# Performance work log

Measured on AMD Instinct MI355X. Metric: run time of the kernel, lower is better.

The kernel has to match this reference:

```python
import jax, jax.numpy as jnp
import numpy as np

N_NODES = 100000
N_EDGES = 2000000
F_IN = 32
HID = 32
N_CLASS = 40


def _gru_cell(m, h, wih, whh, bih, bhh):
    # torch.nn.GRUCell math; wih/whh: [3H, H_in], gates ordered r, z, n
    gi = m @ wih.T + bih
    gh = h @ whh.T + bhh
    i_r, i_z, i_n = jnp.split(gi, 3, axis=-1)
    h_r, h_z, h_n = jnp.split(gh, 3, axis=-1)
    r = jax.nn.sigmoid(i_r + h_r)
    z = jax.nn.sigmoid(i_z + h_z)
    n = jnp.tanh(i_n + r * h_n)
    return (1.0 - z) * n + z * h


def _gated_conv(x, edge_index, edge_weight, w_proj, w_msg, wih, whh, bih, bhh):
    h = x @ w_proj                                   # [N, out]
    msg = (h @ w_msg)[edge_index[0]] * edge_weight[:, None]  # gather src -> [E, out]
    agg = jax.ops.segment_sum(msg, edge_index[1], num_segments=N_NODES)  # scatter-add to dst
    return _gru_cell(agg, h, wih, whh, bih, bhh)


def setup_inputs() -> dict:
    key = jax.random.key(0)
    ks = jax.random.split(key, 16)
    s = 0.1
    return {
        "x": jax.random.normal(ks[0], (N_NODES, F_IN), jnp.float32),
        "edge_index": jax.random.randint(ks[1], (2, N_EDGES), 0, N_NODES, jnp.int64),
        "edge_weight": jax.random.uniform(ks[2], (N_EDGES,), jnp.float32),
        "W1_proj": jax.random.normal(ks[3], (F_IN, HID), jnp.float32) * s,
        "W1_msg": jax.random.normal(ks[4], (HID, HID), jnp.float32) * s,
        "gru1_wih": jax.random.normal(ks[5], (3 * HID, HID), jnp.float32) * s,
        "gru1_whh": jax.random.normal(ks[6], (3 * HID, HID), jnp.float32) * s,
        "gru1_bih": jax.random.normal(ks[7], (3 * HID,), jnp.float32) * s,
        "gru1_bhh": jax.random.normal(ks[8], (3 * HID,), jnp.float32) * s,
        "W2_proj": jax.random.normal(ks[9], (HID, N_CLASS), jnp.float32) * s,
        "W2_msg": jax.random.normal(ks[10], (N_CLASS, N_CLASS), jnp.float32) * s,
        "gru2_wih": jax.random.normal(ks[11], (3 * N_CLASS, N_CLASS), jnp.float32) * s,
        "gru2_whh": jax.random.normal(ks[12], (3 * N_CLASS, N_CLASS), jnp.float32) * s,
        "gru2_bih": jax.random.normal(ks[13], (3 * N_CLASS,), jnp.float32) * s,
        "gru2_bhh": jax.random.normal(ks[14], (3 * N_CLASS,), jnp.float32) * s,
    }


def reference(x, edge_index, edge_weight, W1_proj, W1_msg, gru1_wih, gru1_whh,
              gru1_bih, gru1_bhh, W2_proj, W2_msg, gru2_wih, gru2_whh,
              gru2_bih, gru2_bhh):
    # eval mode: dropout is identity
    h = _gated_conv(x, edge_index, edge_weight, W1_proj, W1_msg,
                    gru1_wih, gru1_whh, gru1_bih, gru1_bhh)
    h = jax.nn.relu(h)
    h = _gated_conv(h, edge_index, edge_weight, W2_proj, W2_msg,
                    gru2_wih, gru2_whh, gru2_bih, gru2_bhh)
    return jax.nn.log_softmax(h, axis=-1)
```

## Files before the change

### kernel.cpp

```cpp
#include <hip/hip_runtime.h>
#include <math.h>

#define NN 100000
#define NP 100032
#define NE 2000000
#define FIN 32
#define H 32
#define NC 40

#define NBK 196
#define BSH 9
#define CAP 10880
#define EPT 16
#define EPB (256 * EPT)

#define NPROJ 12500
#define NWB 104

typedef _Float16 half_t;
typedef __attribute__((ext_vector_type(8))) _Float16 half8;
typedef __attribute__((ext_vector_type(4))) float f32x4;
typedef long long ll2 __attribute__((ext_vector_type(2)));

__device__ __forceinline__ float sigm_(float x) {
    return 1.0f / (1.0f + __expf(-x));
}
__device__ __forceinline__ float tanh_(float x) {
    x = fminf(fmaxf(x, -20.0f), 20.0f);
    float e = __expf(2.0f * x);
    return (e - 1.0f) / (e + 1.0f);
}

__device__ __forceinline__ void agg_run(int n, int q,
                                        const int* __restrict__ ofs,
                                        const int* __restrict__ ocn,
                                        const int2* __restrict__ evs,
                                        const half_t* __restrict__ src,
                                        float* acc) {
    const half8* s8 = (const half8*)src + q;
    const long long* ev8 = (const long long*)evs;
    int e = ofs[n];
    int e1 = e + ocn[n];
    if ((e & 1) && e < e1) {
        long long r = __builtin_nontemporal_load(ev8 + e);
        float w = __int_as_float((int)(r >> 32));
        half8 hv = s8[(size_t)(r & 0x1FFFF) * 4];
#pragma unroll
        for (int t = 0; t < 8; ++t) acc[t] += w * (float)hv[t];
        ++e;
    }
    for (; e + 8 <= e1; e += 8) {
        ll2 p0 = __builtin_nontemporal_load((const ll2*)(ev8 + e));
        ll2 p1 = __builtin_nontemporal_load((const ll2*)(ev8 + e + 2));
        ll2 p2 = __builtin_nontemporal_load((const ll2*)(ev8 + e + 4));
        ll2 p3 = __builtin_nontemporal_load((const ll2*)(ev8 + e + 6));
        half8 h0 = s8[(size_t)(p0[0] & 0x1FFFF) * 4];
        half8 h1 = s8[(size_t)(p0[1] & 0x1FFFF) * 4];
        half8 h2 = s8[(size_t)(p1[0] & 0x1FFFF) * 4];
        half8 h3 = s8[(size_t)(p1[1] & 0x1FFFF) * 4];
        half8 h4 = s8[(size_t)(p2[0] & 0x1FFFF) * 4];
        half8 h5 = s8[(size_t)(p2[1] & 0x1FFFF) * 4];
        half8 h6 = s8[(size_t)(p3[0] & 0x1FFFF) * 4];
        half8 h7 = s8[(size_t)(p3[1] & 0x1FFFF) * 4];
        float w0 = __int_as_float((int)(p0[0] >> 32));
        float w1 = __int_as_float((int)(p0[1] >> 32));
        float w2 = __int_as_float((int)(p1[0] >> 32));
        float w3 = __int_as_float((int)(p1[1] >> 32));
        float w4 = __int_as_float((int)(p2[0] >> 32));
        float w5 = __int_as_float((int)(p2[1] >> 32));
        float w6 = __int_as_float((int)(p3[0] >> 32));
        float w7 = __int_as_float((int)(p3[1] >> 32));
#pragma unroll
        for (int t = 0; t < 8; ++t) {
            acc[t] += w0 * (float)h0[t];
            acc[t] += w1 * (float)h1[t];
            acc[t] += w2 * (float)h2[t];
            acc[t] += w3 * (float)h3[t];
            acc[t] += w4 * (float)h4[t];
            acc[t] += w5 * (float)h5[t];
            acc[t] += w6 * (float)h6[t];
            acc[t] += w7 * (float)h7[t];
        }
    }
    if (e + 4 <= e1) {
        ll2 p0 = __builtin_nontemporal_load((const ll2*)(ev8 + e));
        ll2 p1 = __builtin_nontemporal_load((const ll2*)(ev8 + e + 2));
        half8 h0 = s8[(size_t)(p0[0] & 0x1FFFF) * 4];
        half8 h1 = s8[(size_t)(p0[1] & 0x1FFFF) * 4];
        half8 h2 = s8[(size_t)(p1[0] & 0x1FFFF) * 4];
        half8 h3 = s8[(size_t)(p1[1] & 0x1FFFF) * 4];
        float w0 = __int_as_float((int)(p0[0] >> 32));
        float w1 = __int_as_float((int)(p0[1] >> 32));
        float w2 = __int_as_float((int)(p1[0] >> 32));
        float w3 = __int_as_float((int)(p1[1] >> 32));
#pragma unroll
        for (int t = 0; t < 8; ++t) {
            acc[t] += w0 * (float)h0[t];
            acc[t] += w1 * (float)h1[t];
            acc[t] += w2 * (float)h2[t];
            acc[t] += w3 * (float)h3[t];
        }
        e += 4;
    }
    if (e + 2 <= e1) {
        ll2 p0 = __builtin_nontemporal_load((const ll2*)(ev8 + e));
        half8 h0 = s8[(size_t)(p0[0] & 0x1FFFF) * 4];
        half8 h1 = s8[(size_t)(p0[1] & 0x1FFFF) * 4];
        float w0 = __int_as_float((int)(p0[0] >> 32));
        float w1 = __int_as_float((int)(p0[1] >> 32));
#pragma unroll
        for (int t = 0; t < 8; ++t) {
            acc[t] += w0 * (float)h0[t];
            acc[t] += w1 * (float)h1[t];
        }
        e += 2;
    }
    if (e < e1) {
        long long r = __builtin_nontemporal_load(ev8 + e);
        float w = __int_as_float((int)(r >> 32));
        half8 hv = s8[(size_t)(r & 0x1FFFF) * 4];
#pragma unroll
        for (int t = 0; t < 8; ++t) acc[t] += w * (float)hv[t];
    }
}

__global__ __launch_bounds__(256) void kA_bucket(const int* __restrict__ ei,
                                                 const float* __restrict__ ew,
                                                 int* __restrict__ gcur,
                                                 long long* __restrict__ rec) {
    __shared__ long long recs[EPB];
    __shared__ int gdst[EPB];
    __shared__ int cnt[NBK], base[NBK], sofs[NBK];
    __shared__ int ssc[256];
    int tid = threadIdx.x;
    for (int i = tid; i < NBK; i += 256) cnt[i] = 0;
    __syncthreads();
    int e0 = blockIdx.x * EPB;
    int dcache[EPT];
#pragma unroll
    for (int i = 0; i < EPT; ++i) {
        int e = e0 + i * 256 + tid;
        dcache[i] = (e < NE) ? ei[NE + e] : -1;
        if (e < NE) atomicAdd(&cnt[dcache[i] >> BSH], 1);
    }
    __syncthreads();
    int cv = (tid < NBK) ? cnt[tid] : 0;
    ssc[tid] = cv;
    __syncthreads();
    for (int off = 1; off < 256; off <<= 1) {
        int v = (tid >= off) ? ssc[tid - off] : 0;
        __syncthreads();
        ssc[tid] += v;
        __syncthreads();
    }
    if (tid < NBK) {
        sofs[tid] = ssc[tid] - cv;
        base[tid] = atomicAdd(&gcur[tid], cv);
        cnt[tid] = 0;
    }
    __syncthreads();
#pragma unroll
    for (int i = 0; i < EPT; ++i) {
        int e = e0 + i * 256 + tid;
        if (e < NE) {
            int d = dcache[i], s = ei[e];
            int b = d >> BSH;
            int r = atomicAdd(&cnt[b], 1);
            int slot = sofs[b] + r;
            int pos = base[b] + r;
            int lo = s | ((d & 511) << 17);
            recs[slot] = (long long)(unsigned)lo |
                         ((long long)__float_as_int(ew[e]) << 32);
            gdst[slot] = (pos < CAP) ? (b * CAP + pos) : -1;
        }
    }
    __syncthreads();
    int nrec = min(EPB, NE - e0);
    for (int i = tid; i < nrec; i += 256) {
        int gd = gdst[i];
        if (gd >= 0) rec[gd] = recs[i];
    }
}

__global__ __launch_bounds__(256) void kB_sort(const int* __restrict__ gcur,
                                               const int2* __restrict__ rec,
                                               int2* __restrict__ evs,
                                               int* __restrict__ ofs,
                                               int* __restrict__ ocn) {
    __shared__ int hist[2048], lofs[2048], ssc[256];
    int tid = threadIdx.x, b = blockIdx.x;
    int nb0 = b << BSH;
    int nnodes = min(512, NN - nb0);
    int cntb = min(gcur[b], CAP);
    for (int i = tid; i < 2048; i += 256) hist[i] = 0;
    __syncthreads();
    const int2* rb = rec + (size_t)b * CAP;
    for (int i = tid; i < cntb; i += 256) {
        int rx = rb[i].x;
        int bin = (((rx >> 17) & 511) << 2) | ((rx & 0x1FFFF) >> 15);
        atomicAdd(&hist[bin], 1);
    }
    __syncthreads();
    int base = tid * 8, ls = 0, lh[8];
#pragma unroll
    for (int j = 0; j < 8; ++j) {
        lh[j] = hist[base + j];
        ls += lh[j];
    }
    ssc[tid] = ls;
    __syncthreads();
    for (int off = 1; off < 256; off <<= 1) {
        int v = (tid >= off) ? ssc[tid - off] : 0;
        __syncthreads();
        ssc[tid] += v;
        __syncthreads();
    }
    int ex = ssc[tid] - ls;
#pragma unroll
    for (int j = 0; j < 8; ++j) {
        lofs[base + j] = ex;
        ex += lh[j];
    }
    __syncthreads();
    for (int l = tid; l < nnodes; l += 256) {
        int c = hist[4 * l] + hist[4 * l + 1] + hist[4 * l + 2] + hist[4 * l + 3];
        ofs[nb0 + l] = b * CAP + lofs[4 * l];
        ocn[nb0 + l] = c;
    }
    __syncthreads();
    for (int i = tid; i < 2048; i += 256) hist[i] = 0;
    __syncthreads();
    int2* eb = evs + (size_t)b * CAP;
    for (int i = tid; i < cntb; i += 256) {
        int2 r = rb[i];
        int bin = (((r.x >> 17) & 511) << 2) | ((r.x & 0x1FFFF) >> 15);
        int rk = atomicAdd(&hist[bin], 1);
        eb[lofs[bin] + rk] = make_int2(r.x & 0x1FFFF, r.y);
    }
}

__global__ __launch_bounds__(256) void k_prep(const float* __restrict__ x,
                                              const float* __restrict__ W1p,
                                              const float* __restrict__ W1m,
                                              const float* __restrict__ wih1,
                                              const float* __restrict__ whh1,
                                              const float* __restrict__ W2p,
                                              const float* __restrict__ W2m,
                                              const float* __restrict__ wih2,
                                              const float* __restrict__ whh2,
                                              half_t* __restrict__ Hd,
                                              half_t* __restrict__ W1sw,
                                              half_t* __restrict__ W2sw,
                                              int* __restrict__ gcur) {
    __shared__ float sWp[FIN * H];
    __shared__ float sx[8][FIN];
    __shared__ float P2l[32 * NC];
    int b = blockIdx.x, tid = threadIdx.x;
    if (b < NPROJ) {
        for (int i = tid; i < FIN * H; i += 256) sWp[i] = W1p[i];
        int nb = b * 8;
        int nl = tid >> 5, j = tid & 31;
        int n = nb + nl;
        if (n < NN) sx[nl][j] = x[(size_t)n * FIN + j];
        __syncthreads();
        float acc = 0.f;
#pragma unroll
        for (int k = 0; k < FIN; ++k) acc += sx[nl][k] * sWp[k * H + j];
        if (n < NN) Hd[(size_t)n * 32 + j] = (half_t)acc;
        return;
    }
    int wb = b - NPROJ;
    if (wb == 0 && tid < NBK) gcur[tid] = 0;
    int i = wb * 256 + tid;
    if (i < 8192) {
        int j = i & 7, lane = (i >> 3) & 63, ct = (i >> 9) & 7, s = i >> 12;
        int k = s * 32 + (lane >> 4) * 8 + j;
        int col = ct * 16 + (lane & 15);
        int g = col >> 5, jj = col & 31;
        float v = 0.f;
        if (g <= 2) {
            if (k < 32) {
                float acc = 0.f;
#pragma unroll
                for (int t = 0; t < H; ++t) acc += W1m[k * H + t] * wih1[(g * H + jj) * H + t];
                v = acc;
            } else if (g < 2) {
                v = whh1[(g * H + jj) * H + (k - 32)];
            }
        } else {
            if (k >= 32) v = whh1[(2 * H + jj) * H + (k - 32)];
        }
        W1sw[i] = (half_t)v;
    } else {
        for (int e = tid; e < 32 * NC; e += 256) {
            int k = e / NC, t = e % NC;
            float a = 0.f;
#pragma unroll
            for (int u = 0; u < NC; ++u) a += W2p[k * NC + u] * W2m[u * NC + t];
            P2l[e] = a;
        }
        __syncthreads();
        int i2 = i - 8192;
        int j = i2 & 7, lane = (i2 >> 3) & 63;
        int tt = i2 >> 9;
        int ct = tt % 12, s = tt / 12;
        int k = s * 32 + (lane >> 4) * 8 + j;
        int col = ct * 16 + (lane & 15);
        int g = col / 48, jj = col % 48;
        float v = 0.f;
        if (jj < NC) {
            if (g <= 2) {
                if (k < 32) {
                    float acc = 0.f;
#pragma unroll
                    for (int t = 0; t < NC; ++t)
                        acc += P2l[k * NC + t] * wih2[(g * NC + jj) * NC + t];
                    v = acc;
                } else if (k < 72 && g < 2) {
                    v = whh2[(g * NC + jj) * NC + (k - 32)];
                }
            } else {
                if (k >= 32 && k < 72) v = whh2[(2 * NC + jj) * NC + (k - 32)];
            }
        }
        W2sw[i2] = (half_t)v;
    }
}

__global__ __launch_bounds__(256) void k_l1(const int* __restrict__ ofs,
                                            const int* __restrict__ ocn,
                                            const int2* __restrict__ evs,
                                            const half_t* __restrict__ Hd,
                                            const half8* __restrict__ W1sw,
                                            const float* __restrict__ bih,
                                            const float* __restrict__ bhh,
                                            half_t* __restrict__ Hh) {
    __shared__ half8 aggT[64][4];
    __shared__ half8 hd8[64][4];
    int tid = threadIdx.x;
    int nl = tid >> 2, q = tid & 3;
    int n = blockIdx.x * 64 + nl;
    half8 hz;
#pragma unroll
    for (int t = 0; t < 8; ++t) hz[t] = (half_t)0.f;
    hd8[nl][q] = (n < NN) ? ((const half8*)Hd)[(size_t)n * 4 + q] : hz;
    float acc[8] = {0.f, 0.f, 0.f, 0.f, 0.f, 0.f, 0.f, 0.f};
    if (n < NN) agg_run(n, q, ofs, ocn, evs, Hd, acc);
    half8 o;
#pragma unroll
    for (int t = 0; t < 8; ++t) o[t] = (half_t)acc[t];
    aggT[nl][q] = o;
    __syncthreads();
    int wave = tid >> 6, lane = tid & 63;
    int m16 = lane & 15, qq = lane >> 4;
    int nbw = blockIdx.x * 64 + wave * 16;
    half8 a0 = aggT[wave * 16 + m16][qq];
    half8 a1 = hd8[wave * 16 + m16][qq];
    f32x4 macc[8];
#pragma unroll
    for (int ct = 0; ct < 8; ++ct) macc[ct] = (f32x4){0.f, 0.f, 0.f, 0.f};
#pragma unroll
    for (int ct = 0; ct < 8; ++ct) {
        macc[ct] = __builtin_amdgcn_mfma_f32_16x16x32_f16(a0, W1sw[ct * 64 + lane], macc[ct], 0, 0, 0);
        macc[ct] = __builtin_amdgcn_mfma_f32_16x16x32_f16(a1, W1sw[(8 + ct) * 64 + lane], macc[ct], 0, 0, 0);
    }
#pragma unroll
    for (int ct = 0; ct < 2; ++ct) {
        int j = ct * 16 + m16;
        float br = bih[j] + bhh[j];
        float bz = bih[H + j] + bhh[H + j];
        float bi = bih[2 * H + j], bh = bhh[2 * H + j];
#pragma unroll
        for (int m = 0; m < 4; ++m) {
            int node = nbw + qq * 4 + m;
            float r = sigm_(macc[ct][m] + br);
            float z = sigm_(macc[2 + ct][m] + bz);
            float ng = tanh_(macc[4 + ct][m] + bi + r * (macc[6 + ct][m] + bh));
            float hj = (float)hd8[wave * 16 + qq * 4 + m][j >> 3][j & 7];
            float out = fmaxf((1.f - z) * ng + z * hj, 0.f);
            if (node < NN) Hh[(size_t)node * 32 + j] = (half_t)out;
        }
    }
}

__global__ __launch_bounds__(256) void k_l2(const int* __restrict__ ofs,
                                            const int* __restrict__ ocn,
                                            const int2* __restrict__ evs,
                                            const half_t* __restrict__ Hh,
                                            const half8* __restrict__ W2sw,
                                            const float* __restrict__ W2p,
                                            const float* __restrict__ bih,
                                            const float* __restrict__ bhh,
                                            float* __restrict__ out) {
    __shared__ half8 aggT[64][4];
    __shared__ half8 hh8[64][4];
    __shared__ half8 h2c8[64][8];
    __shared__ float sW[FIN * NC];
    int tid = threadIdx.x;
    int nl = tid >> 2, q = tid & 3;
    int n = blockIdx.x * 64 + nl;
    for (int i = tid; i < FIN * NC; i += 256) sW[i] = W2p[i];
    half8 hz;
#pragma unroll
    for (int t = 0; t < 8; ++t) hz[t] = (half_t)0.f;
    hh8[nl][q] = (n < NN) ? ((const half8*)Hh)[(size_t)n * 4 + q] : hz;
    float acc[8] = {0.f, 0.f, 0.f, 0.f, 0.f, 0.f, 0.f, 0.f};
    if (n < NN) agg_run(n, q, ofs, ocn, evs, Hh, acc);
    half8 o;
#pragma unroll
    for (int t = 0; t < 8; ++t) o[t] = (half_t)acc[t];
    aggT[nl][q] = o;
    __syncthreads();
    {
        half8 hr[4];
#pragma unroll
        for (int t = 0; t < 4; ++t) hr[t] = hh8[nl][t];
        half_t* h2row = (half_t*)h2c8[nl];
        float a[10];
#pragma unroll
        for (int j0 = 0; j0 < 10; ++j0) a[j0] = 0.f;
#pragma unroll
        for (int k = 0; k < FIN; ++k) {
            float hk = (float)hr[k >> 3][k & 7];
#pragma unroll
            for (int j0 = 0; j0 < 10; ++j0) a[j0] += hk * sW[k * NC + q * 10 + j0];
        }
#pragma unroll
        for (int j0 = 0; j0 < 10; ++j0) h2row[q * 10 + j0] = (half_t)a[j0];
#pragma unroll
        for (int j0 = 0; j0 < 6; ++j0) h2row[40 + q * 6 + j0] = (half_t)0.f;
    }
    __syncthreads();
    int wave = tid >> 6, lane = tid & 63;
    int m16 = lane & 15, qq = lane >> 4;
    int nbw = blockIdx.x * 64 + wave * 16;
    half8 a0 = aggT[wave * 16 + m16][qq];
    half8 a1 = h2c8[wave * 16 + m16][qq];
    half8 a2 = h2c8[wave * 16 + m16][4 + qq];
    f32x4 macc[12];
#pragma unroll
    for (int ct = 0; ct < 12; ++ct) macc[ct] = (f32x4){0.f, 0.f, 0.f, 0.f};
#pragma unroll
    for (int ct = 0; ct < 12; ++ct) {
        macc[ct] = __builtin_amdgcn_mfma_f32_16x16x32_f16(a0, W2sw[ct * 64 + lane], macc[ct], 0, 0, 0);
        macc[ct] = __builtin_amdgcn_mfma_f32_16x16x32_f16(a1, W2sw[(12 + ct) * 64 + lane], macc[ct], 0, 0, 0);
        macc[ct] = __builtin_amdgcn_mfma_f32_16x16x32_f16(a2, W2sw[(24 + ct) * 64 + lane], macc[ct], 0, 0, 0);
    }
    float v[3][4];
#pragma unroll
    for (int ct = 0; ct < 3; ++ct) {
        int j = ct * 16 + m16;
        int jc = (j < NC) ? j : (NC - 1);
        float br = bih[jc] + bhh[jc];
        float bz = bih[NC + jc] + bhh[NC + jc];
        float bi = bih[2 * NC + jc], bh = bhh[2 * NC + jc];
#pragma unroll
        for (int m = 0; m < 4; ++m) {
            float r = sigm_(macc[ct][m] + br);
            float z = sigm_(macc[3 + ct][m] + bz);
            float ng = tanh_(macc[6 + ct][m] + bi + r * (macc[9 + ct][m] + bh));
            float hj = (float)((const half_t*)h2c8[wave * 16 + qq * 4 + m])[jc];
            v[ct][m] = (1.f - z) * ng + z * hj;
        }
    }
    bool v2ok = (m16 < 8);
#pragma unroll
    for (int m = 0; m < 4; ++m) {
        float mx = fmaxf(v[0][m], v[1][m]);
        if (v2ok) mx = fmaxf(mx, v[2][m]);
#pragma unroll
        for (int d = 1; d < 16; d <<= 1) mx = fmaxf(mx, __shfl_xor(mx, d));
        float se = __expf(v[0][m] - mx) + __expf(v[1][m] - mx) +
                   (v2ok ? __expf(v[2][m] - mx) : 0.f);
#pragma unroll
        for (int d = 1; d < 16; d <<= 1) se += __shfl_xor(se, d);
        float ls = mx + __logf(se);
        int node = nbw + qq * 4 + m;
        if (node < NN) {
            out[(size_t)node * NC + m16] = v[0][m] - ls;
            out[(size_t)node * NC + 16 + m16] = v[1][m] - ls;
            if (v2ok) out[(size_t)node * NC + 32 + m16] = v[2][m] - ls;
        }
    }
}

extern "C" void kernel_launch(void* const* d_in, const int* in_sizes, int n_in,
                              void* d_out, int out_size, void* d_ws, size_t ws_size,
                              hipStream_t stream) {
    const float* x = (const float*)d_in[0];
    const int* ei = (const int*)d_in[1];
    const float* ew = (const float*)d_in[2];
    const float* W1p = (const float*)d_in[3];
    const float* W1m = (const float*)d_in[4];
    const float* g1wih = (const float*)d_in[5];
    const float* g1whh = (const float*)d_in[6];
    const float* g1bih = (const float*)d_in[7];
    const float* g1bhh = (const float*)d_in[8];
    const float* W2p = (const float*)d_in[9];
    const float* W2m = (const float*)d_in[10];
    const float* g2wih = (const float*)d_in[11];
    const float* g2whh = (const float*)d_in[12];
    const float* g2bih = (const float*)d_in[13];
    const float* g2bhh = (const float*)d_in[14];
    float* ws = (float*)d_ws;

    long long* rec = (long long*)ws;
    int2* evs = (int2*)(ws + 4264960);
    half_t* Hd = (half_t*)(ws + 8529920);
    half_t* Hh = (half_t*)(ws + 10130176);
    int* ofs = (int*)(ws + 11730432);
    int* ocn = (int*)(ws + 11830432);
    int* gcur = (int*)(ws + 11930432);
    half_t* W1sw = (half_t*)(ws + 11930688);
    half_t* W2sw = W1sw + 8192;
    float* out = (float*)d_out;

    k_prep<<<NPROJ + NWB, 256, 0, stream>>>(x, W1p, W1m, g1wih, g1whh,
                                            W2p, W2m, g2wih, g2whh,
                                            Hd, W1sw, W2sw, gcur);
    kA_bucket<<<(NE + EPB - 1) / EPB, 256, 0, stream>>>(ei, ew, gcur, rec);
    kB_sort<<<NBK, 256, 0, stream>>>(gcur, (const int2*)rec, evs, ofs, ocn);
    k_l1<<<NP / 64, 256, 0, stream>>>(ofs, ocn, evs, Hd, (const half8*)W1sw,
                                      g1bih, g1bhh, Hh);
    k_l2<<<NP / 64, 256, 0, stream>>>(ofs, ocn, evs, Hh, (const half8*)W2sw,
                                      W2p, g2bih, g2bhh, out);
}
```

Baseline: 278.4 us.

## Aggregate in MFMA lane layout and extract h via identity weight columns

The GRU kernels now run the edge aggregation directly in the MFMA operand layout, with each lane owning node m16 and quarter qq. This removes the shared-memory staging of aggregates and node features along with the __syncthreads barriers. The hidden-state value needed for the GRU blend is recovered in the accumulator layout by appending identity blocks to the swizzled weight matrices, which adds extra MFMA column tiles (10 instead of 8, 15 instead of 12). In layer 2 the per-node projection is computed per lane in registers, with lane group 0 doing the extra 8 columns.

Result: slower. 371.0 us (+33.3%).

```diff
diff --git a/kernel.cpp b/kernel.cpp
--- a/kernel.cpp
+++ b/kernel.cpp
@@ -15,7 +15,9 @@
 #define EPB (256 * EPT)
 
 #define NPROJ 12500
-#define NWB 104
+#define NCT1 10
+#define NCT2 15
+#define NWB 130
 
 typedef _Float16 half_t;
 typedef __attribute__((ext_vector_type(8))) _Float16 half8;
@@ -271,9 +273,11 @@
     }
     int wb = b - NPROJ;
     if (wb == 0 && tid < NBK) gcur[tid] = 0;
-    int i = wb * 256 + tid;
-    if (i < 8192) {
-        int j = i & 7, lane = (i >> 3) & 63, ct = (i >> 9) & 7, s = i >> 12;
+    if (wb < 40) {
+        int i = wb * 256 + tid;
+        int j = i & 7, lane = (i >> 3) & 63;
+        int rest = i >> 9;
+        int ct = rest % NCT1, s = rest / NCT1;
         int k = s * 32 + (lane >> 4) * 8 + j;
         int col = ct * 16 + (lane & 15);
         int g = col >> 5, jj = col & 31;
@@ -287,8 +291,10 @@
             } else if (g < 2) {
                 v = whh1[(g * H + jj) * H + (k - 32)];
             }
+        } else if (g == 3) {
+            if (k >= 32) v = whh1[(2 * H + jj) * H + (k - 32)];
         } else {
-            if (k >= 32) v = whh1[(2 * H + jj) * H + (k - 32)];
+            if (k >= 32 && (k - 32) == jj) v = 1.f;
         }
         W1sw[i] = (half_t)v;
     } else {
@@ -300,10 +306,10 @@
             P2l[e] = a;
         }
         __syncthreads();
-        int i2 = i - 8192;
+        int i2 = (wb - 40) * 256 + tid;
         int j = i2 & 7, lane = (i2 >> 3) & 63;
-        int tt = i2 >> 9;
-        int ct = tt % 12, s = tt / 12;
+        int rest = i2 >> 9;
+        int ct = rest % NCT2, s = rest / NCT2;
         int k = s * 32 + (lane >> 4) * 8 + j;
         int col = ct * 16 + (lane & 15);
         int g = col / 48, jj = col % 48;
@@ -319,8 +325,10 @@
                 } else if (k < 72 && g < 2) {
                     v = whh2[(g * NC + jj) * NC + (k - 32)];
                 }
+            } else if (g == 3) {
+                if (k >= 32 && k < 72) v = whh2[(2 * NC + jj) * NC + (k - 32)];
             } else {
-                if (k >= 32 && k < 72) v = whh2[(2 * NC + jj) * NC + (k - 32)];
+                if (k >= 32 && k < 72 && (k - 32) == jj) v = 1.f;
             }
         }
         W2sw[i2] = (half_t)v;
@@ -335,34 +343,27 @@
                                             const float* __restrict__ bih,
                                             const float* __restrict__ bhh,
                                             half_t* __restrict__ Hh) {
-    __shared__ half8 aggT[64][4];
-    __shared__ half8 hd8[64][4];
     int tid = threadIdx.x;
-    int nl = tid >> 2, q = tid & 3;
-    int n = blockIdx.x * 64 + nl;
-    half8 hz;
-#pragma unroll
-    for (int t = 0; t < 8; ++t) hz[t] = (half_t)0.f;
-    hd8[nl][q] = (n < NN) ? ((const half8*)Hd)[(size_t)n * 4 + q] : hz;
-    float acc[8] = {0.f, 0.f, 0.f, 0.f, 0.f, 0.f, 0.f, 0.f};
-    if (n < NN) agg_run(n, q, ofs, ocn, evs, Hd, acc);
-    half8 o;
-#pragma unroll
-    for (int t = 0; t < 8; ++t) o[t] = (half_t)acc[t];
-    aggT[nl][q] = o;
-    __syncthreads();
     int wave = tid >> 6, lane = tid & 63;
     int m16 = lane & 15, qq = lane >> 4;
     int nbw = blockIdx.x * 64 + wave * 16;
-    half8 a0 = aggT[wave * 16 + m16][qq];
-    half8 a1 = hd8[wave * 16 + m16][qq];
-    f32x4 macc[8];
-#pragma unroll
-    for (int ct = 0; ct < 8; ++ct) macc[ct] = (f32x4){0.f, 0.f, 0.f, 0.f};
-#pragma unroll
-    for (int ct = 0; ct < 8; ++ct) {
+    int n = nbw + m16;
+    half8 a1;
+#pragma unroll
+    for (int t = 0; t < 8; ++t) a1[t] = (half_t)0.f;
+    if (n < NN) a1 = ((const half8*)Hd)[(size_t)n * 4 + qq];
+    float acc[8] = {0.f, 0.f, 0.f, 0.f, 0.f, 0.f, 0.f, 0.f};
+    if (n < NN) agg_run(n, qq, ofs, ocn, evs, Hd, acc);
+    half8 a0;
+#pragma unroll
+    for (int t = 0; t < 8; ++t) a0[t] = (half_t)acc[t];
+    f32x4 macc[NCT1];
+#pragma unroll
+    for (int ct = 0; ct < NCT1; ++ct) macc[ct] = (f32x4){0.f, 0.f, 0.f, 0.f};
+#pragma unroll
+    for (int ct = 0; ct < NCT1; ++ct) {
         macc[ct] = __builtin_amdgcn_mfma_f32_16x16x32_f16(a0, W1sw[ct * 64 + lane], macc[ct], 0, 0, 0);
-        macc[ct] = __builtin_amdgcn_mfma_f32_16x16x32_f16(a1, W1sw[(8 + ct) * 64 + lane], macc[ct], 0, 0, 0);
+        macc[ct] = __builtin_amdgcn_mfma_f32_16x16x32_f16(a1, W1sw[(NCT1 + ct) * 64 + lane], macc[ct], 0, 0, 0);
     }
 #pragma unroll
     for (int ct = 0; ct < 2; ++ct) {
@@ -376,9 +377,9 @@
             float r = sigm_(macc[ct][m] + br);
             float z = sigm_(macc[2 + ct][m] + bz);
             float ng = tanh_(macc[4 + ct][m] + bi + r * (macc[6 + ct][m] + bh));
-            float hj = (float)hd8[wave * 16 + qq * 4 + m][j >> 3][j & 7];
-            float out = fmaxf((1.f - z) * ng + z * hj, 0.f);
-            if (node < NN) Hh[(size_t)node * 32 + j] = (half_t)out;
+            float hj = macc[8 + ct][m];
+            float o = fmaxf((1.f - z) * ng + z * hj, 0.f);
+            if (node < NN) Hh[(size_t)node * 32 + j] = (half_t)o;
         }
     }
 }
@@ -392,59 +393,58 @@
                                             const float* __restrict__ bih,
                                             const float* __restrict__ bhh,
                                             float* __restrict__ out) {
-    __shared__ half8 aggT[64][4];
-    __shared__ half8 hh8[64][4];
-    __shared__ half8 h2c8[64][8];
     __shared__ float sW[FIN * NC];
     int tid = threadIdx.x;
-    int nl = tid >> 2, q = tid & 3;
-    int n = blockIdx.x * 64 + nl;
-    for (int i = tid; i < FIN * NC; i += 256) sW[i] = W2p[i];
-    half8 hz;
-#pragma unroll
-    for (int t = 0; t < 8; ++t) hz[t] = (half_t)0.f;
-    hh8[nl][q] = (n < NN) ? ((const half8*)Hh)[(size_t)n * 4 + q] : hz;
-    float acc[8] = {0.f, 0.f, 0.f, 0.f, 0.f, 0.f, 0.f, 0.f};
-    if (n < NN) agg_run(n, q, ofs, ocn, evs, Hh, acc);
-    half8 o;
-#pragma unroll
-    for (int t = 0; t < 8; ++t) o[t] = (half_t)acc[t];
-    aggT[nl][q] = o;
-    __syncthreads();
-    {
-        half8 hr[4];
-#pragma unroll
-        for (int t = 0; t < 4; ++t) hr[t] = hh8[nl][t];
-        half_t* h2row = (half_t*)h2c8[nl];
-        float a[10];
-#pragma unroll
-        for (int j0 = 0; j0 < 10; ++j0) a[j0] = 0.f;
-#pragma unroll
-        for (int k = 0; k < FIN; ++k) {
-            float hk = (float)hr[k >> 3][k & 7];
-#pragma unroll
-            for (int j0 = 0; j0 < 10; ++j0) a[j0] += hk * sW[k * NC + q * 10 + j0];
-        }
-#pragma unroll
-        for (int j0 = 0; j0 < 10; ++j0) h2row[q * 10 + j0] = (half_t)a[j0];
-#pragma unroll
-        for (int j0 = 0; j0 < 6; ++j0) h2row[40 + q * 6 + j0] = (half_t)0.f;
-    }
-    __syncthreads();
     int wave = tid >> 6, lane = tid & 63;
     int m16 = lane & 15, qq = lane >> 4;
     int nbw = blockIdx.x * 64 + wave * 16;
-    half8 a0 = aggT[wave * 16 + m16][qq];
-    half8 a1 = h2c8[wave * 16 + m16][qq];
-    half8 a2 = h2c8[wave * 16 + m16][4 + qq];
-    f32x4 macc[12];
-#pragma unroll
-    for (int ct = 0; ct < 12; ++ct) macc[ct] = (f32x4){0.f, 0.f, 0.f, 0.f};
-#pragma unroll
-    for (int ct = 0; ct < 12; ++ct) {
+    int n = nbw + m16;
+    for (int i = tid; i < FIN * NC; i += 256) sW[i] = W2p[i];
+    half8 hr[4];
+#pragma unroll
+    for (int t = 0; t < 4; ++t)
+#pragma unroll
+        for (int u = 0; u < 8; ++u) hr[t][u] = (half_t)0.f;
+    if (n < NN) {
+#pragma unroll
+        for (int t = 0; t < 4; ++t) hr[t] = ((const half8*)Hh)[(size_t)n * 4 + t];
+    }
+    __syncthreads();
+    float a1f[8] = {0.f, 0.f, 0.f, 0.f, 0.f, 0.f, 0.f, 0.f};
+    float a2f[8] = {0.f, 0.f, 0.f, 0.f, 0.f, 0.f, 0.f, 0.f};
+#pragma unroll
+    for (int k = 0; k < FIN; ++k) {
+        float hk = (float)hr[k >> 3][k & 7];
+#pragma unroll
+        for (int j0 = 0; j0 < 8; ++j0) a1f[j0] += hk * sW[k * NC + qq * 8 + j0];
+    }
+    if (qq == 0) {
+#pragma unroll
+        for (int k = 0; k < FIN; ++k) {
+            float hk = (float)hr[k >> 3][k & 7];
+#pragma unroll
+            for (int j0 = 0; j0 < 8; ++j0) a2f[j0] += hk * sW[k * NC + 32 + j0];
+        }
+    }
+    half8 a1, a2;
+#pragma unroll
+    for (int t = 0; t < 8; ++t) {
+        a1[t] = (half_t)a1f[t];
+        a2[t] = (half_t)a2f[t];
+    }
+    float acc[8] = {0.f, 0.f, 0.f, 0.f, 0.f, 0.f, 0.f, 0.f};
+    if (n < NN) agg_run(n, qq, ofs, ocn, evs, Hh, acc);
+    half8 a0;
+#pragma unroll
+    for (int t = 0; t < 8; ++t) a0[t] = (half_t)acc[t];
+    f32x4 macc[NCT2];
+#pragma unroll
+    for (int ct = 0; ct < NCT2; ++ct) macc[ct] = (f32x4){0.f, 0.f, 0.f, 0.f};
+#pragma unroll
+    for (int ct = 0; ct < NCT2; ++ct) {
         macc[ct] = __builtin_amdgcn_mfma_f32_16x16x32_f16(a0, W2sw[ct * 64 + lane], macc[ct], 0, 0, 0);
-        macc[ct] = __builtin_amdgcn_mfma_f32_16x16x32_f16(a1, W2sw[(12 + ct) * 64 + lane], macc[ct], 0, 0, 0);
-        macc[ct] = __builtin_amdgcn_mfma_f32_16x16x32_f16(a2, W2sw[(24 + ct) * 64 + lane], macc[ct], 0, 0, 0);
+        macc[ct] = __builtin_amdgcn_mfma_f32_16x16x32_f16(a1, W2sw[(NCT2 + ct) * 64 + lane], macc[ct], 0, 0, 0);
+        macc[ct] = __builtin_amdgcn_mfma_f32_16x16x32_f16(a2, W2sw[(2 * NCT2 + ct) * 64 + lane], macc[ct], 0, 0, 0);
     }
     float v[3][4];
 #pragma unroll
@@ -459,7 +459,7 @@
             float r = sigm_(macc[ct][m] + br);
             float z = sigm_(macc[3 + ct][m] + bz);
             float ng = tanh_(macc[6 + ct][m] + bi + r * (macc[9 + ct][m] + bh));
-            float hj = (float)((const half_t*)h2c8[wave * 16 + qq * 4 + m])[jc];
+            float hj = macc[12 + ct][m];
             v[ct][m] = (1.f - z) * ng + z * hj;
         }
     }
@@ -512,7 +512,7 @@
     int* ocn = (int*)(ws + 11830432);
     int* gcur = (int*)(ws + 11930432);
     half_t* W1sw = (half_t*)(ws + 11930688);
-    half_t* W2sw = W1sw + 8192;
+    half_t* W2sw = W1sw + 10240;
     float* out = (float*)d_out;
 
     k_prep<<<NPROJ + NWB, 256, 0, stream>>>(x, W1p, W1m, g1wih, g1whh,
```
